# Kernel tuning notes

Measured on AMD Instinct MI355X. Metric: run time of the kernel, lower is better.

The kernel has to match this reference:

```python
import jax, jax.numpy as jnp
import numpy as np

B, S, T = 32, 2048, 768
NH, DH, DHID = 8, 96, 384  # num_heads, head_dim, hidden_dim=4*head_dim


def setup_inputs() -> dict:
    key = jax.random.key(0)
    k = jax.random.split(key, 7)
    token_embeddings = jax.random.normal(k[0], (B, S, T), dtype=jnp.float32)
    attention_mask = jnp.ones((B, S), dtype=jnp.float32)
    # per-head Linear params, stacked on a leading head axis (PyTorch default-ish init scale)
    P_w = jax.random.normal(k[1], (NH, T, DH), dtype=jnp.float32) * (1.0 / np.sqrt(T))
    P_b = jax.random.normal(k[2], (NH, DH), dtype=jnp.float32) * 0.01
    W1_w = jax.random.normal(k[3], (NH, DH, DHID), dtype=jnp.float32) * (1.0 / np.sqrt(DH))
    W1_b = jax.random.normal(k[4], (NH, DHID), dtype=jnp.float32) * 0.01
    W2_w = jax.random.normal(k[5], (NH, DHID, DH), dtype=jnp.float32) * (1.0 / np.sqrt(DHID))
    W2_b = jax.random.normal(k[6], (NH, DH), dtype=jnp.float32) * 0.01
    return {
        'token_embeddings': token_embeddings,
        'attention_mask': attention_mask,
        'P_w': P_w, 'P_b': P_b,
        'W1_w': W1_w, 'W1_b': W1_b,
        'W2_w': W2_w, 'W2_b': W2_b,
    }


def reference(token_embeddings, attention_mask, P_w, P_b, W1_w, W1_b, W2_w, W2_b):
    # Batched over heads instead of the original Python loop; same math per head.
    # H_i = P_i(H): (B, NH, S, DH)
    Hi = jnp.einsum('bst,htd->bhsd', token_embeddings, P_w) + P_b[None, :, None, :]
    # A_i = W2_i(relu(W1_i(H_i))): (B, NH, S, DH)
    A = jax.nn.relu(jnp.einsum('bhsd,hde->bhse', Hi, W1_w) + W1_b[None, :, None, :])
    A = jnp.einsum('bhse,hed->bhsd', A, W2_w) + W2_b[None, :, None, :]
    # masked softmax over the sequence axis (log(mask) adds -inf at padded tokens)
    log_mask = jnp.log(attention_mask)[:, None, :, None]  # (B,1,S,1)
    A = jax.nn.softmax(A + log_mask, axis=2)
    # weighted sum over tokens: (B, NH, DH)
    v = jnp.sum(Hi * A, axis=2)
    # concat heads -> (B, NH*DH) == (B, sentence_dim)
    return v.reshape(v.shape[0], NH * DH)
```

## Files before the change

### kernel.cpp

```cpp
#include <hip/hip_runtime.h>
#include <cstdint>
#include <cstddef>

#define Bsz   32
#define Ssz   2048
#define Tsz   768
#define NH    8
#define DH    96
#define DHID  384
#define Ncols (NH*DH)

using u16 = unsigned short;
typedef __bf16 bf16x8 __attribute__((ext_vector_type(8)));
typedef __bf16 bf16x4 __attribute__((ext_vector_type(4)));
typedef float  f32x4  __attribute__((ext_vector_type(4)));

__device__ __forceinline__ u16 f2bn(float f) {
  __bf16 h = (__bf16)f;
  return __builtin_bit_cast(u16, h);
}
__device__ __forceinline__ float b2f(u16 u) {
  return __builtin_bit_cast(float, (uint32_t)u << 16);
}

typedef const __attribute__((address_space(1))) void* gas_t;
typedef __attribute__((address_space(3))) void* las_t;
__device__ __forceinline__ void gload16(const void* g, void* s) {
  __builtin_amdgcn_global_load_lds((gas_t)g, (las_t)s, 16, 0, 0);
}

__global__ __launch_bounds__(256) void k_cvt(const float* __restrict__ e,
                                             u16* __restrict__ o)
{
  size_t t = (size_t)blockIdx.x * 256 + threadIdx.x;
  #pragma unroll
  for (int it = 0; it < 3; ++it) {
    size_t i = (t + (size_t)it * 2097152) * 8;
    float4 v0 = *reinterpret_cast<const float4*>(e + i);
    float4 v1 = *reinterpret_cast<const float4*>(e + i + 4);
    bf16x8 p;
    p[0] = (__bf16)v0.x; p[1] = (__bf16)v0.y; p[2] = (__bf16)v0.z; p[3] = (__bf16)v0.w;
    p[4] = (__bf16)v1.x; p[5] = (__bf16)v1.y; p[6] = (__bf16)v1.z; p[7] = (__bf16)v1.w;
    *reinterpret_cast<bf16x8*>(o + i) = p;
  }
}

__global__ __launch_bounds__(256) void k_pack(const float* __restrict__ Pw,
    const float* __restrict__ W1w, const float* __restrict__ W2w,
    u16* __restrict__ B1t, u16* __restrict__ W1f, u16* __restrict__ W2f)
{
  int i = blockIdx.x * 256 + threadIdx.x;
  if (i < 589824) {
    int n = i / 768, k = i % 768;
    int h = n / 96, d = n % 96;
    B1t[i] = f2bn(Pw[(size_t)h*73728 + (size_t)k*96 + d]);
  } else if (i < 589824 + 294912) {
    int j = i - 589824;
    int h = j / 36864, r = j % 36864;
    int CI = r / 8, e = r % 8;
    int lane = CI % 64, ci2 = CI / 64;
    int ks = ci2 % 3, ct2 = ci2 / 3;
    int t = ct2 % 2, c = ct2 / 2;
    int l15 = lane & 15, lg = lane >> 4;
    int n = c*32 + t*16 + l15;
    int k = ks*32 + lg*8 + e;
    W1f[j] = f2bn(W1w[(size_t)h*36864 + (size_t)k*384 + n]);
  } else if (i < 589824 + 2*294912) {
    int q = i - 589824 - 294912;
    int h = q / 36864, r = q % 36864;
    int CI = r / 8, e = r % 8;
    int lane = CI % 64, ci2 = CI / 64;
    int ct = ci2 % 6, c = ci2 / 6;
    int l15 = lane & 15, lg = lane >> 4;
    int n = ct*16 + l15;
    int k = c*32 + lg*8 + e;
    W2f[q] = f2bn(W2w[(size_t)h*36864 + (size_t)k*96 + n]);
  }
}

__global__ __launch_bounds__(256) void k_gemm1(const u16* __restrict__ embb,
    const u16* __restrict__ B1t, const float* __restrict__ Pb, u16* __restrict__ Hi)
{
  __shared__ u16 As[128*64];
  __shared__ u16 Bs[128*64];
  const int tid  = threadIdx.x;
  const int lane = tid & 63;
  const int w    = tid >> 6;
  const int wr = w >> 1, wc = w & 1;
  const int L = blockIdx.x;
  const int widx = (L & 7) * 384 + (L >> 3);
  const int bm = widx / 6, bn = widx % 6;
  const int l15 = lane & 15, lg = lane >> 4;

  const int lrow = lane >> 3;
  const int lchk = (lane & 7) ^ lrow;

  f32x4 acc[4][4] = {};

  #pragma unroll 1
  for (int kt = 0; kt < 12; ++kt) {
    const int k0 = kt * 64;
    #pragma unroll
    for (int i = 0; i < 4; ++i) {
      const int r8 = (w*4 + i)*8;
      gload16(embb + (size_t)(bm*128 + r8 + lrow)*Tsz + k0 + lchk*8,
              &As[r8*64]);
      gload16(B1t  + (size_t)(bn*128 + r8 + lrow)*Tsz + k0 + lchk*8,
              &Bs[r8*64]);
    }
    __syncthreads();

    __builtin_amdgcn_s_setprio(1);
    #pragma unroll
    for (int kk = 0; kk < 2; ++kk) {
      const int clog = kk*4 + lg;
      bf16x8 b[4];
      #pragma unroll
      for (int c = 0; c < 4; ++c) {
        const int Rb = wc*64 + c*16 + l15;
        b[c] = *reinterpret_cast<const bf16x8*>(&Bs[Rb*64 + (clog ^ (Rb & 7))*8]);
      }
      bf16x8 a[4];
      #pragma unroll
      for (int m = 0; m < 4; ++m) {
        const int R = wr*64 + m*16 + l15;
        a[m] = *reinterpret_cast<const bf16x8*>(&As[R*64 + (clog ^ (R & 7))*8]);
      }
      #pragma unroll
      for (int m = 0; m < 4; ++m)
        #pragma unroll
        for (int c = 0; c < 4; ++c)
          acc[m][c] = __builtin_amdgcn_mfma_f32_16x16x32_bf16(a[m], b[c], acc[m][c], 0, 0, 0);
    }
    __builtin_amdgcn_s_setprio(0);
    __syncthreads();
  }

  #pragma unroll
  for (int c = 0; c < 4; ++c) {
    int col = bn*128 + wc*64 + c*16 + l15;
    float bias = Pb[col];
    #pragma unroll
    for (int m = 0; m < 4; ++m) {
      int row0 = bm*128 + wr*64 + m*16 + lg*4;
      #pragma unroll
      for (int j = 0; j < 4; ++j)
        Hi[(size_t)(row0 + j)*Ncols + col] = f2bn(acc[m][c][j] + bias);
    }
  }
}

__global__ __launch_bounds__(256, 2) void k_gemm1_fb(const float* __restrict__ emb,
    const u16* __restrict__ B1t, const float* __restrict__ Pb, u16* __restrict__ Hi)
{
  __shared__ u16 As[2][128*64];
  __shared__ u16 Bs[2][128*64];
  const int tid  = threadIdx.x;
  const int lane = tid & 63;
  const int w    = tid >> 6;
  const int wr = w >> 1, wc = w & 1;
  const int L = blockIdx.x;
  const int widx = (L & 7) * 384 + (L >> 3);
  const int bm = widx / 6, bn = widx % 6;
  const int l15 = lane & 15, lg = lane >> 4;

  const int srow   = lane >> 3;
  const int schunk = lane & 7;
  const int wchunk = schunk ^ srow;

  bf16x8 pa[4];
  bf16x8 pb[4];

  auto load_tile = [&](int kt) {
    const int k0 = kt * 64;
    #pragma unroll
    for (int i = 0; i < 4; ++i) {
      const int row = w*32 + i*8 + srow;
      const float* src = emb + (size_t)(bm*128 + row)*Tsz + k0 + schunk*8;
      float4 v0 = *reinterpret_cast<const float4*>(src);
      float4 v1 = *reinterpret_cast<const float4*>(src + 4);
      bf16x8 af;
      af[0] = (__bf16)v0.x; af[1] = (__bf16)v0.y; af[2] = (__bf16)v0.z; af[3] = (__bf16)v0.w;
      af[4] = (__bf16)v1.x; af[5] = (__bf16)v1.y; af[6] = (__bf16)v1.z; af[7] = (__bf16)v1.w;
      pa[i] = af;
    }
    #pragma unroll
    for (int i = 0; i < 4; ++i) {
      const int row = w*32 + i*8 + srow;
      pb[i] = *reinterpret_cast<const bf16x8*>(
          B1t + (size_t)(bn*128 + row)*Tsz + k0 + schunk*8);
    }
  };
  auto write_tile = [&](int buf) {
    #pragma unroll
    for (int i = 0; i < 4; ++i) {
      const int row = w*32 + i*8 + srow;
      *reinterpret_cast<bf16x8*>(&As[buf][row*64 + wchunk*8]) = pa[i];
      *reinterpret_cast<bf16x8*>(&Bs[buf][row*64 + wchunk*8]) = pb[i];
    }
  };

  f32x4 acc[4][4] = {};

  load_tile(0);
  write_tile(0);
  __syncthreads();

  #pragma unroll 1
  for (int kt = 0; kt < 12; ++kt) {
    const int cur = kt & 1;
    if (kt < 11) load_tile(kt + 1);
    __builtin_amdgcn_s_setprio(1);
    #pragma unroll
    for (int kk = 0; kk < 2; ++kk) {
      const int clog = kk*4 + lg;
      bf16x8 b[4];
      #pragma unroll
      for (int c = 0; c < 4; ++c) {
        const int Rb = wc*64 + c*16 + l15;
        b[c] = *reinterpret_cast<const bf16x8*>(&Bs[cur][Rb*64 + (clog ^ (Rb & 7))*8]);
      }
      bf16x8 a[4];
      #pragma unroll
      for (int m = 0; m < 4; ++m) {
        const int R = wr*64 + m*16 + l15;
        a[m] = *reinterpret_cast<const bf16x8*>(&As[cur][R*64 + (clog ^ (R & 7))*8]);
      }
      #pragma unroll
      for (int m = 0; m < 4; ++m)
        #pragma unroll
        for (int c = 0; c < 4; ++c)
          acc[m][c] = __builtin_amdgcn_mfma_f32_16x16x32_bf16(a[m], b[c], acc[m][c], 0, 0, 0);
    }
    __builtin_amdgcn_s_setprio(0);
    if (kt < 11) write_tile(cur ^ 1);
    __syncthreads();
  }

  #pragma unroll
  for (int c = 0; c < 4; ++c) {
    int col = bn*128 + wc*64 + c*16 + l15;
    float bias = Pb[col];
    #pragma unroll
    for (int m = 0; m < 4; ++m) {
      int row0 = bm*128 + wr*64 + m*16 + lg*4;
      #pragma unroll
      for (int j = 0; j < 4; ++j)
        Hi[(size_t)(row0 + j)*Ncols + col] = f2bn(acc[m][c][j] + bias);
    }
  }
}

__global__ __launch_bounds__(512, 1) void k_ffn_pool(
    const u16* __restrict__ Hi, const u16* __restrict__ W1f, const u16* __restrict__ W2f,
    const float* __restrict__ b1, const float* __restrict__ b2v, const float* __restrict__ mask,
    float* __restrict__ out)
{
  __shared__ u16 W1s[36864];
  __shared__ u16 W2s[36864];
  __shared__ u16 Zb[8][16][40];

  const int tid = threadIdx.x, lane = tid & 63, w = tid >> 6;
  const int l15 = lane & 15, lg = lane >> 4;
  const int h = blockIdx.x, b = blockIdx.y;

  const u16* W1h = W1f + (size_t)h * DHID * DH;
  const u16* W2h = W2f + (size_t)h * DH * DHID;
  const float* b1h = b1 + h * DHID;

  for (int i = tid; i < 4608; i += 512) {
    *reinterpret_cast<uint4*>(&W1s[i*8]) = *reinterpret_cast<const uint4*>(W1h + i*8);
    *reinterpret_cast<uint4*>(&W2s[i*8]) = *reinterpret_cast<const uint4*>(W2h + i*8);
  }
  __syncthreads();

  float b2s[6];
  #pragma unroll
  for (int ct = 0; ct < 6; ++ct) b2s[ct] = b2v[h*DH + ct*16 + l15];

  float Mr[6], Lr[6], Ar[6];
  #pragma unroll
  for (int ct = 0; ct < 6; ++ct) { Mr[ct] = -3.4e38f; Lr[ct] = 0.f; Ar[ct] = 0.f; }

  #pragma unroll 1
  for (int pass = 0; pass < 4; ++pass) {
    const size_t prow = (size_t)b*Ssz + (size_t)w*256 + (size_t)pass*64;

    bf16x8 hifr[4][3];
    #pragma unroll
    for (int s = 0; s < 4; ++s)
      #pragma unroll
      for (int ks = 0; ks < 3; ++ks)
        hifr[s][ks] = *reinterpret_cast<const bf16x8*>(
            Hi + (prow + s*16 + l15)*Ncols + h*DH + ks*32 + lg*8);

    f32x4 lgt[4][6] = {};

    #pragma unroll 2
    for (int c = 0; c < 12; ++c) {
      bf16x8 a1c[2][3];
      #pragma unroll
      for (int t = 0; t < 2; ++t)
        #pragma unroll
        for (int ks = 0; ks < 3; ++ks)
          a1c[t][ks] = *reinterpret_cast<const bf16x8*>(
              &W1s[(((c*2 + t)*3 + ks)*64 + lane)*8]);
      float4 bc0 = *reinterpret_cast<const float4*>(b1h + c*32 + lg*4);
      float4 bc1 = *reinterpret_cast<const float4*>(b1h + c*32 + 16 + lg*4);
      bf16x8 b2fr[6];
      #pragma unroll
      for (int ct = 0; ct < 6; ++ct)
        b2fr[ct] = *reinterpret_cast<const bf16x8*>(
            &W2s[((c*6 + ct)*64 + lane)*8]);

      #pragma unroll
      for (int s = 0; s < 4; ++s) {
        f32x4 z0 = {}, z1 = {};
        #pragma unroll
        for (int ks = 0; ks < 3; ++ks) {
          z0 = __builtin_amdgcn_mfma_f32_16x16x32_bf16(a1c[0][ks], hifr[s][ks], z0, 0, 0, 0);
          z1 = __builtin_amdgcn_mfma_f32_16x16x32_bf16(a1c[1][ks], hifr[s][ks], z1, 0, 0, 0);
        }
        bf16x4 p0, p1;
        p0[0] = (__bf16)fmaxf(z0[0] + bc0.x, 0.f);
        p0[1] = (__bf16)fmaxf(z0[1] + bc0.y, 0.f);
        p0[2] = (__bf16)fmaxf(z0[2] + bc0.z, 0.f);
        p0[3] = (__bf16)fmaxf(z0[3] + bc0.w, 0.f);
        p1[0] = (__bf16)fmaxf(z1[0] + bc1.x, 0.f);
        p1[1] = (__bf16)fmaxf(z1[1] + bc1.y, 0.f);
        p1[2] = (__bf16)fmaxf(z1[2] + bc1.z, 0.f);
        p1[3] = (__bf16)fmaxf(z1[3] + bc1.w, 0.f);
        *reinterpret_cast<uint2*>(&Zb[w][l15][lg*4])      = __builtin_bit_cast(uint2, p0);
        *reinterpret_cast<uint2*>(&Zb[w][l15][16 + lg*4]) = __builtin_bit_cast(uint2, p1);
        bf16x8 zf = *reinterpret_cast<const bf16x8*>(&Zb[w][l15][lg*8]);
        #pragma unroll
        for (int ct = 0; ct < 6; ++ct)
          lgt[s][ct] = __builtin_amdgcn_mfma_f32_16x16x32_bf16(zf, b2fr[ct], lgt[s][ct], 0, 0, 0);
      }
    }

    float lmv[4][4];
    #pragma unroll
    for (int s = 0; s < 4; ++s) {
      float4 mk = *reinterpret_cast<const float4*>(&mask[prow + s*16 + lg*4]);
      lmv[s][0] = __logf(mk.x); lmv[s][1] = __logf(mk.y);
      lmv[s][2] = __logf(mk.z); lmv[s][3] = __logf(mk.w);
    }
    float G[4][6][4];
    #pragma unroll
    for (int s = 0; s < 4; ++s)
      #pragma unroll
      for (int ct = 0; ct < 6; ++ct)
        #pragma unroll
        for (int j = 0; j < 4; ++j)
          G[s][ct][j] = b2f(Hi[(prow + s*16 + lg*4 + j)*Ncols + h*DH + ct*16 + l15]);

    #pragma unroll
    for (int ct = 0; ct < 6; ++ct) {
      float av[4][4];
      float m16 = -3.4e38f;
      #pragma unroll
      for (int s = 0; s < 4; ++s)
        #pragma unroll
        for (int j = 0; j < 4; ++j) {
          av[s][j] = lgt[s][ct][j] + b2s[ct] + lmv[s][j];
          m16 = fmaxf(m16, av[s][j]);
        }
      m16 = fmaxf(m16, __shfl_xor(m16, 16));
      m16 = fmaxf(m16, __shfl_xor(m16, 32));
      float l16 = 0.f, a16 = 0.f;
      #pragma unroll
      for (int s = 0; s < 4; ++s)
        #pragma unroll
        for (int j = 0; j < 4; ++j) {
          float p = __expf(av[s][j] - m16);
          l16 += p;
          a16 += p * G[s][ct][j];
        }
      l16 += __shfl_xor(l16, 16); l16 += __shfl_xor(l16, 32);
      a16 += __shfl_xor(a16, 16); a16 += __shfl_xor(a16, 32);
      float M2 = fmaxf(Mr[ct], m16);
      float eo = __expf(Mr[ct] - M2), en = __expf(m16 - M2);
      Lr[ct] = Lr[ct]*eo + l16*en;
      Ar[ct] = Ar[ct]*eo + a16*en;
      Mr[ct] = M2;
    }
  }

  float* mw = reinterpret_cast<float*>(&Zb[w][0][0]);
  if (lane < 16) {
    #pragma unroll
    for (int ct = 0; ct < 6; ++ct) {
      mw[      ct*16 + l15] = Mr[ct];
      mw[ 96 + ct*16 + l15] = Lr[ct];
      mw[192 + ct*16 + l15] = Ar[ct];
    }
  }
  __syncthreads();
  if (tid < 96) {
    float m = -3.4e38f;
    #pragma unroll
    for (int q = 0; q < 8; ++q) {
      const float* mq = reinterpret_cast<const float*>(&Zb[q][0][0]);
      m = fmaxf(m, mq[tid]);
    }
    float l = 0.f, a = 0.f;
    #pragma unroll
    for (int q = 0; q < 8; ++q) {
      const float* mq = reinterpret_cast<const float*>(&Zb[q][0][0]);
      float sc = __expf(mq[tid] - m);
      l += mq[96 + tid] * sc;
      a += mq[192 + tid] * sc;
    }
    out[(size_t)b * Ncols + h*DH + tid] = a / l;
  }
}

extern "C" void kernel_launch(void* const* d_in, const int* in_sizes, int n_in,
                              void* d_out, int out_size, void* d_ws, size_t ws_size,
                              hipStream_t stream)
{
  const float* emb  = (const float*)d_in[0];
  const float* mask = (const float*)d_in[1];
  const float* Pw   = (const float*)d_in[2];
  const float* Pb   = (const float*)d_in[3];
  const float* W1w  = (const float*)d_in[4];
  const float* W1b  = (const float*)d_in[5];
  const float* W2w  = (const float*)d_in[6];
  const float* W2b  = (const float*)d_in[7];
  float* out = (float*)d_out;

  char* ws = (char*)d_ws;
  if (ws_size >= 203685888ull) {
    u16* embb = (u16*)(ws);
    u16* Hi   = (u16*)(ws + 100663296ull);
    u16* B1t  = (u16*)(ws + 201326592ull);
    u16* W1f  = (u16*)(ws + 202506240ull);
    u16* W2f  = (u16*)(ws + 203096064ull);
    k_cvt <<<dim3(8192), dim3(256), 0, stream>>>(emb, embb);
    k_pack<<<dim3(4608), dim3(256), 0, stream>>>(Pw, W1w, W2w, B1t, W1f, W2f);
    k_gemm1<<<dim3(3072), dim3(256), 0, stream>>>(embb, B1t, Pb, Hi);
    k_ffn_pool<<<dim3(8, 32), dim3(512), 0, stream>>>(Hi, W1f, W2f, W1b, W2b, mask, out);
  } else {
    u16* Hi  = (u16*)(ws);
    u16* B1t = (u16*)(ws + 100663296ull);
    u16* W1f = (u16*)(ws + 101842944ull);
    u16* W2f = (u16*)(ws + 102432768ull);
    k_pack<<<dim3(4608), dim3(256), 0, stream>>>(Pw, W1w, W2w, B1t, W1f, W2f);
    k_gemm1_fb<<<dim3(3072), dim3(256), 0, stream>>>(emb, B1t, Pb, Hi);
    k_ffn_pool<<<dim3(8, 32), dim3(512), 0, stream>>>(Hi, W1f, W2f, W1b, W2b, mask, out);
  }
}
```

Baseline: 254.5 us.

## Double-buffer LDS tiles in gemm1 and merge convert and pack kernels

The projection GEMM now keeps two LDS buffers per operand. The global-to-LDS loads for tile k+1 are issued before the MFMA work on tile k, so the per-tile barrier-then-load stall is hidden behind compute. This doubles per-block LDS to 64KB, which may lower how many blocks fit on a CU. Separately, the fp32→bf16 embedding conversion and the weight-packing kernels are fused into a single launch with block-range dispatch, saving one kernel launch and its tail.

Result: slower. 262.5 us (+3.1%).

```diff
diff --git a/kernel.cpp b/kernel.cpp
--- a/kernel.cpp
+++ b/kernel.cpp
@@ -29,19 +29,51 @@
   __builtin_amdgcn_global_load_lds((gas_t)g, (las_t)s, 16, 0, 0);
 }
 
-__global__ __launch_bounds__(256) void k_cvt(const float* __restrict__ e,
-                                             u16* __restrict__ o)
-{
-  size_t t = (size_t)blockIdx.x * 256 + threadIdx.x;
-  #pragma unroll
-  for (int it = 0; it < 3; ++it) {
-    size_t i = (t + (size_t)it * 2097152) * 8;
-    float4 v0 = *reinterpret_cast<const float4*>(e + i);
-    float4 v1 = *reinterpret_cast<const float4*>(e + i + 4);
-    bf16x8 p;
-    p[0] = (__bf16)v0.x; p[1] = (__bf16)v0.y; p[2] = (__bf16)v0.z; p[3] = (__bf16)v0.w;
-    p[4] = (__bf16)v1.x; p[5] = (__bf16)v1.y; p[6] = (__bf16)v1.z; p[7] = (__bf16)v1.w;
-    *reinterpret_cast<bf16x8*>(o + i) = p;
+__global__ __launch_bounds__(256) void k_cvtpack(const float* __restrict__ e,
+    u16* __restrict__ o, const float* __restrict__ Pw,
+    const float* __restrict__ W1w, const float* __restrict__ W2w,
+    u16* __restrict__ B1t, u16* __restrict__ W1f, u16* __restrict__ W2f)
+{
+  if (blockIdx.x < 8192) {
+    size_t t = (size_t)blockIdx.x * 256 + threadIdx.x;
+    #pragma unroll
+    for (int it = 0; it < 3; ++it) {
+      size_t i = (t + (size_t)it * 2097152) * 8;
+      float4 v0 = *reinterpret_cast<const float4*>(e + i);
+      float4 v1 = *reinterpret_cast<const float4*>(e + i + 4);
+      bf16x8 p;
+      p[0] = (__bf16)v0.x; p[1] = (__bf16)v0.y; p[2] = (__bf16)v0.z; p[3] = (__bf16)v0.w;
+      p[4] = (__bf16)v1.x; p[5] = (__bf16)v1.y; p[6] = (__bf16)v1.z; p[7] = (__bf16)v1.w;
+      *reinterpret_cast<bf16x8*>(o + i) = p;
+    }
+    return;
+  }
+  int i = (blockIdx.x - 8192) * 256 + threadIdx.x;
+  if (i < 589824) {
+    int n = i / 768, k = i % 768;
+    int h = n / 96, d = n % 96;
+    B1t[i] = f2bn(Pw[(size_t)h*73728 + (size_t)k*96 + d]);
+  } else if (i < 589824 + 294912) {
+    int j = i - 589824;
+    int h = j / 36864, r = j % 36864;
+    int CI = r / 8, el = r % 8;
+    int lane = CI % 64, ci2 = CI / 64;
+    int ks = ci2 % 3, ct2 = ci2 / 3;
+    int t = ct2 % 2, c = ct2 / 2;
+    int l15 = lane & 15, lg = lane >> 4;
+    int n = c*32 + t*16 + l15;
+    int k = ks*32 + lg*8 + el;
+    W1f[j] = f2bn(W1w[(size_t)h*36864 + (size_t)k*384 + n]);
+  } else if (i < 589824 + 2*294912) {
+    int q = i - 589824 - 294912;
+    int h = q / 36864, r = q % 36864;
+    int CI = r / 8, el = r % 8;
+    int lane = CI % 64, ci2 = CI / 64;
+    int ct = ci2 % 6, c = ci2 / 6;
+    int l15 = lane & 15, lg = lane >> 4;
+    int n = ct*16 + l15;
+    int k = c*32 + lg*8 + el;
+    W2f[q] = f2bn(W2w[(size_t)h*36864 + (size_t)k*96 + n]);
   }
 }
 
@@ -57,23 +89,23 @@
   } else if (i < 589824 + 294912) {
     int j = i - 589824;
     int h = j / 36864, r = j % 36864;
-    int CI = r / 8, e = r % 8;
+    int CI = r / 8, el = r % 8;
     int lane = CI % 64, ci2 = CI / 64;
     int ks = ci2 % 3, ct2 = ci2 / 3;
     int t = ct2 % 2, c = ct2 / 2;
     int l15 = lane & 15, lg = lane >> 4;
     int n = c*32 + t*16 + l15;
-    int k = ks*32 + lg*8 + e;
+    int k = ks*32 + lg*8 + el;
     W1f[j] = f2bn(W1w[(size_t)h*36864 + (size_t)k*384 + n]);
   } else if (i < 589824 + 2*294912) {
     int q = i - 589824 - 294912;
     int h = q / 36864, r = q % 36864;
-    int CI = r / 8, e = r % 8;
+    int CI = r / 8, el = r % 8;
     int lane = CI % 64, ci2 = CI / 64;
     int ct = ci2 % 6, c = ci2 / 6;
     int l15 = lane & 15, lg = lane >> 4;
     int n = ct*16 + l15;
-    int k = c*32 + lg*8 + e;
+    int k = c*32 + lg*8 + el;
     W2f[q] = f2bn(W2w[(size_t)h*36864 + (size_t)k*96 + n]);
   }
 }
@@ -81,8 +113,8 @@
 __global__ __launch_bounds__(256) void k_gemm1(const u16* __restrict__ embb,
     const u16* __restrict__ B1t, const float* __restrict__ Pb, u16* __restrict__ Hi)
 {
-  __shared__ u16 As[128*64];
-  __shared__ u16 Bs[128*64];
+  __shared__ u16 As[2][128*64];
+  __shared__ u16 Bs[2][128*64];
   const int tid  = threadIdx.x;
   const int lane = tid & 63;
   const int w    = tid >> 6;
@@ -95,20 +127,27 @@
   const int lrow = lane >> 3;
   const int lchk = (lane & 7) ^ lrow;
 
-  f32x4 acc[4][4] = {};
-
-  #pragma unroll 1
-  for (int kt = 0; kt < 12; ++kt) {
+  auto stage = [&](int kt, int buf) {
     const int k0 = kt * 64;
     #pragma unroll
     for (int i = 0; i < 4; ++i) {
       const int r8 = (w*4 + i)*8;
       gload16(embb + (size_t)(bm*128 + r8 + lrow)*Tsz + k0 + lchk*8,
-              &As[r8*64]);
+              &As[buf][r8*64]);
       gload16(B1t  + (size_t)(bn*128 + r8 + lrow)*Tsz + k0 + lchk*8,
-              &Bs[r8*64]);
-    }
-    __syncthreads();
+              &Bs[buf][r8*64]);
+    }
+  };
+
+  f32x4 acc[4][4] = {};
+
+  stage(0, 0);
+  __syncthreads();
+
+  #pragma unroll 1
+  for (int kt = 0; kt < 12; ++kt) {
+    const int cur = kt & 1;
+    if (kt < 11) stage(kt + 1, cur ^ 1);
 
     __builtin_amdgcn_s_setprio(1);
     #pragma unroll
@@ -118,13 +157,13 @@
       #pragma unroll
       for (int c = 0; c < 4; ++c) {
         const int Rb = wc*64 + c*16 + l15;
-        b[c] = *reinterpret_cast<const bf16x8*>(&Bs[Rb*64 + (clog ^ (Rb & 7))*8]);
+        b[c] = *reinterpret_cast<const bf16x8*>(&Bs[cur][Rb*64 + (clog ^ (Rb & 7))*8]);
       }
       bf16x8 a[4];
       #pragma unroll
       for (int m = 0; m < 4; ++m) {
         const int R = wr*64 + m*16 + l15;
-        a[m] = *reinterpret_cast<const bf16x8*>(&As[R*64 + (clog ^ (R & 7))*8]);
+        a[m] = *reinterpret_cast<const bf16x8*>(&As[cur][R*64 + (clog ^ (R & 7))*8]);
       }
       #pragma unroll
       for (int m = 0; m < 4; ++m)
@@ -437,8 +476,7 @@
     u16* B1t  = (u16*)(ws + 201326592ull);
     u16* W1f  = (u16*)(ws + 202506240ull);
     u16* W2f  = (u16*)(ws + 203096064ull);
-    k_cvt <<<dim3(8192), dim3(256), 0, stream>>>(emb, embb);
-    k_pack<<<dim3(4608), dim3(256), 0, stream>>>(Pw, W1w, W2w, B1t, W1f, W2f);
+    k_cvtpack<<<dim3(12800), dim3(256), 0, stream>>>(emb, embb, Pw, W1w, W2w, B1t, W1f, W2f);
     k_gemm1<<<dim3(3072), dim3(256), 0, stream>>>(embb, B1t, Pb, Hi);
     k_ffn_pool<<<dim3(8, 32), dim3(512), 0, stream>>>(Hi, W1f, W2f, W1b, W2b, mask, out);
   } else {
```
